# Kernel tuning notes

Measured on AMD Instinct MI355X. Metric: run time of the kernel, lower is better.

Reference implementation:

```python
import jax, jax.numpy as jnp
import numpy as np

N = 262144       # rows
D = 256          # feature dim
CLUSTER = 512    # number of clusters


def setup_inputs() -> dict:
    key = jax.random.key(0)
    k1, k2 = jax.random.split(key)
    matrix = jax.random.normal(k1, (N, D), dtype=jnp.float32)
    label = jax.random.randint(k2, (N,), 0, CLUSTER, dtype=jnp.int32)
    return {"matrix": matrix, "label": label}


def reference(matrix, label):
    # Segment-mean: scatter-add rows into their cluster, divide by counts.
    # (Intended math of the original per-row loop + count-normalize.)
    sums = jax.ops.segment_sum(matrix, label, num_segments=CLUSTER)            # [C, D]
    counts = jax.ops.segment_sum(
        jnp.ones((matrix.shape[0],), matrix.dtype), label, num_segments=CLUSTER
    )                                                                          # [C]
    centers = sums / jnp.maximum(counts, 1.0)[:, None]                         # [C, D]

    # torch.nn.functional.pdist: L2 distance over all unordered pairs i<j.
    iu, ju = jnp.triu_indices(CLUSTER, k=1)                                    # static [P]
    diff = centers[iu] - centers[ju]                                           # [P, D]
    sq = jnp.sum(diff * diff, axis=-1)                                         # [P]
    dist = jnp.sqrt(jnp.maximum(sq, 1e-12))                                    # eps-guard for sqrt grad
    return -jnp.mean(dist)
```

## Files before the change

### kernel.cpp

```cpp
#include <hip/hip_runtime.h>

#define NROWS   262144
#define DIM     256
#define CLUSTER 512
#define NPAIR   (CLUSTER * (CLUSTER - 1) / 2)
#define G       16
#define CPG     32
#define R       64
#define CHUNK   (NROWS / R)
#define PAIR_BLOCKS 2044

__global__ __launch_bounds__(256) void k_gather(const float* __restrict__ matrix,
                                                const int* __restrict__ label,
                                                float* __restrict__ partial,
                                                int* __restrict__ countpart) {
    int g = blockIdx.x & (G - 1);
    int r = blockIdx.x >> 4;
    int t = threadIdx.x;
    int w = t >> 6, lane = t & 63;
    int base = r * CHUNK;

    __shared__ unsigned short list[CHUNK];
    __shared__ int cnt[CPG];
    __shared__ int off[CPG + 1];
    __shared__ int cur[CPG];

    if (t < CPG) cnt[t] = 0;
    __syncthreads();

    for (int i = t; i < CHUNK; i += 256) {
        int lab = label[base + i];
        if ((lab >> 5) == g) atomicAdd(&cnt[lab & (CPG - 1)], 1);
    }
    __syncthreads();

    if (t == 0) {
        int s = 0;
        #pragma unroll
        for (int c = 0; c < CPG; ++c) { off[c] = s; cur[c] = s; s += cnt[c]; }
        off[CPG] = s;
    }
    __syncthreads();

    for (int i = t; i < CHUNK; i += 256) {
        int lab = label[base + i];
        if ((lab >> 5) == g) {
            int p = atomicAdd(&cur[lab & (CPG - 1)], 1);
            list[p] = (unsigned short)i;
        }
    }
    __syncthreads();

    #pragma unroll
    for (int q = 0; q < 8; ++q) {
        int cl = q * 4 + w;
        int s0 = off[cl], s1 = off[cl + 1];
        float ax = 0.f, ay = 0.f, az = 0.f, aw = 0.f;
        #pragma unroll 4
        for (int k = s0; k < s1; ++k) {
            int li = list[k];
            const float4* row = (const float4*)(matrix + (size_t)(base + li) * DIM);
            float4 v = row[lane];
            ax += v.x; ay += v.y; az += v.z; aw += v.w;
        }
        int c = g * CPG + cl;
        ((float4*)(partial + ((size_t)c * R + r) * DIM))[lane] =
            make_float4(ax, ay, az, aw);
    }
    if (t < CPG) countpart[r * CLUSTER + g * CPG + t] = cnt[t];
}

__global__ __launch_bounds__(256) void k_center(const float* __restrict__ partial,
                                                const int* __restrict__ countpart,
                                                float* __restrict__ centers) {
    int c = blockIdx.x, d = threadIdx.x;
    __shared__ float invc;
    if (d == 0) {
        int s = 0;
        for (int r = 0; r < R; ++r) s += countpart[r * CLUSTER + c];
        invc = 1.0f / (float)max(s, 1);
    }
    float acc = 0.f;
    const float* p = partial + (size_t)c * R * DIM + d;
    #pragma unroll 8
    for (int r = 0; r < R; ++r) acc += p[r * DIM];
    __syncthreads();
    centers[c * DIM + d] = acc * invc;
}

__device__ __forceinline__ long long tri_off(long long i) {
    return i * (2 * CLUSTER - i - 1) / 2;
}

__global__ __launch_bounds__(256) void k_pairs(const float* __restrict__ centers,
                                               float* __restrict__ partials) {
    int wave = threadIdx.x >> 6;
    int lane = threadIdx.x & 63;
    long long base = ((long long)blockIdx.x * 4 + wave) * 16;

    double sq = sqrt((double)((2LL * CLUSTER - 1) * (2LL * CLUSTER - 1) - 8 * base));
    int i = (int)(((2 * CLUSTER - 1) - sq) * 0.5);
    if (i < 0) i = 0;
    while (tri_off(i + 1) <= base) ++i;
    while (tri_off(i) > base) --i;
    int j = (int)(base - tri_off(i)) + i + 1;

    float wsum = 0.f;
    #pragma unroll 4
    for (int q = 0; q < 16; ++q) {
        const float4* ci = (const float4*)(centers + (size_t)i * DIM);
        const float4* cj = (const float4*)(centers + (size_t)j * DIM);
        float4 a = ci[lane], b = cj[lane];
        float dx = a.x - b.x, dy = a.y - b.y, dz = a.z - b.z, dw = a.w - b.w;
        float local = dx * dx + dy * dy + dz * dz + dw * dw;
        #pragma unroll
        for (int o = 32; o; o >>= 1) local += __shfl_xor(local, o, 64);
        wsum += sqrtf(fmaxf(local, 1e-12f));
        if (++j == CLUSTER) { ++i; j = i + 1; }
    }

    __shared__ float bsum[4];
    if (lane == 0) bsum[wave] = wsum;
    __syncthreads();
    if (threadIdx.x == 0)
        partials[blockIdx.x] = bsum[0] + bsum[1] + bsum[2] + bsum[3];
}

__global__ __launch_bounds__(256) void k_final(const float* __restrict__ partials, int nb,
                                               float* __restrict__ out) {
    __shared__ float s[256];
    float acc = 0.f;
    for (int i = threadIdx.x; i < nb; i += 256) acc += partials[i];
    s[threadIdx.x] = acc;
    __syncthreads();
    for (int d = 128; d; d >>= 1) {
        if (threadIdx.x < d) s[threadIdx.x] += s[threadIdx.x + d];
        __syncthreads();
    }
    if (threadIdx.x == 0) out[0] = -s[0] / (float)NPAIR;
}

extern "C" void kernel_launch(void* const* d_in, const int* in_sizes, int n_in,
                              void* d_out, int out_size, void* d_ws, size_t ws_size,
                              hipStream_t stream) {
    const float* matrix = (const float*)d_in[0];
    const int* label = (const int*)d_in[1];
    float* out = (float*)d_out;

    float* partial   = (float*)d_ws;
    float* centers   = partial + (size_t)CLUSTER * R * DIM;
    float* ppart     = centers + (size_t)CLUSTER * DIM;
    int*   countpart = (int*)(ppart + 4096);

    k_gather<<<G * R, 256, 0, stream>>>(matrix, label, partial, countpart);
    k_center<<<CLUSTER, 256, 0, stream>>>(partial, countpart, centers);
    k_pairs<<<PAIR_BLOCKS, 256, 0, stream>>>(centers, ppart);
    k_final<<<1, 256, 0, stream>>>(ppart, PAIR_BLOCKS, out);
}
```

Measured before the change: 402.0 us.

## Replace per-chunk partial sums with global atomic accumulation into cluster sums

The gather kernel now accumulates its per-cluster row sums straight into a global [C,D] buffer with float atomics, instead of writing a [C,R,D] partial array. The separate center reduction kernel becomes a simple elementwise normalize. A memset zeroes the sums and counts first, and empty clusters are skipped. This removes the 32 MB partial write and its re-read, at the cost of atomic contention (64 chunks per address), an extra memset launch, and a summation order that is no longer deterministic.

```diff
diff --git a/kernel.cpp b/kernel.cpp
--- a/kernel.cpp
+++ b/kernel.cpp
@@ -12,8 +12,8 @@
 
 __global__ __launch_bounds__(256) void k_gather(const float* __restrict__ matrix,
                                                 const int* __restrict__ label,
-                                                float* __restrict__ partial,
-                                                int* __restrict__ countpart) {
+                                                float* __restrict__ sums,
+                                                int* __restrict__ counts) {
     int g = blockIdx.x & (G - 1);
     int r = blockIdx.x >> 4;
     int t = threadIdx.x;
@@ -55,6 +55,7 @@
     for (int q = 0; q < 8; ++q) {
         int cl = q * 4 + w;
         int s0 = off[cl], s1 = off[cl + 1];
+        if (s0 == s1) continue;
         float ax = 0.f, ay = 0.f, az = 0.f, aw = 0.f;
         #pragma unroll 4
         for (int k = s0; k < s1; ++k) {
@@ -63,29 +64,24 @@
             float4 v = row[lane];
             ax += v.x; ay += v.y; az += v.z; aw += v.w;
         }
-        int c = g * CPG + cl;
-        ((float4*)(partial + ((size_t)c * R + r) * DIM))[lane] =
-            make_float4(ax, ay, az, aw);
+        float* dst = sums + ((size_t)(g * CPG + cl)) * DIM + lane * 4;
+        atomicAdd(dst + 0, ax);
+        atomicAdd(dst + 1, ay);
+        atomicAdd(dst + 2, az);
+        atomicAdd(dst + 3, aw);
     }
-    if (t < CPG) countpart[r * CLUSTER + g * CPG + t] = cnt[t];
+    if (t < CPG && cnt[t]) atomicAdd(&counts[g * CPG + t], cnt[t]);
 }
 
-__global__ __launch_bounds__(256) void k_center(const float* __restrict__ partial,
-                                                const int* __restrict__ countpart,
-                                                float* __restrict__ centers) {
-    int c = blockIdx.x, d = threadIdx.x;
-    __shared__ float invc;
-    if (d == 0) {
-        int s = 0;
-        for (int r = 0; r < R; ++r) s += countpart[r * CLUSTER + c];
-        invc = 1.0f / (float)max(s, 1);
-    }
-    float acc = 0.f;
-    const float* p = partial + (size_t)c * R * DIM + d;
-    #pragma unroll 8
-    for (int r = 0; r < R; ++r) acc += p[r * DIM];
-    __syncthreads();
-    centers[c * DIM + d] = acc * invc;
+__global__ __launch_bounds__(256) void k_norm(const float* __restrict__ sums,
+                                              const int* __restrict__ counts,
+                                              float* __restrict__ centers) {
+    int idx = blockIdx.x * 256 + threadIdx.x;
+    int c = idx >> 6;
+    float inv = 1.0f / (float)max(counts[c], 1);
+    float4 s = ((const float4*)sums)[idx];
+    s.x *= inv; s.y *= inv; s.z *= inv; s.w *= inv;
+    ((float4*)centers)[idx] = s;
 }
 
 __device__ __forceinline__ long long tri_off(long long i) {
@@ -147,13 +143,15 @@
     const int* label = (const int*)d_in[1];
     float* out = (float*)d_out;
 
-    float* partial   = (float*)d_ws;
-    float* centers   = partial + (size_t)CLUSTER * R * DIM;
-    float* ppart     = centers + (size_t)CLUSTER * DIM;
-    int*   countpart = (int*)(ppart + 4096);
+    float* sums    = (float*)d_ws;
+    int*   counts  = (int*)(sums + (size_t)CLUSTER * DIM);
+    float* centers = (float*)(counts + CLUSTER);
+    float* ppart   = centers + (size_t)CLUSTER * DIM;
 
-    k_gather<<<G * R, 256, 0, stream>>>(matrix, label, partial, countpart);
-    k_center<<<CLUSTER, 256, 0, stream>>>(partial, countpart, centers);
+    hipMemsetAsync(sums, 0, (size_t)CLUSTER * DIM * sizeof(float) + CLUSTER * sizeof(int),
+                   stream);
+    k_gather<<<G * R, 256, 0, stream>>>(matrix, label, sums, counts);
+    k_norm<<<CLUSTER * DIM / 4 / 256, 256, 0, stream>>>(sums, counts, centers);
     k_pairs<<<PAIR_BLOCKS, 256, 0, stream>>>(centers, ppart);
     k_final<<<1, 256, 0, stream>>>(ppart, PAIR_BLOCKS, out);
 }
```

Result: slower. 565.3 us (+40.6%).

## Software-prefetch gathered rows, vectorize label scans, fold final reduction into atomics

Applied to the files above, without the earlier changes.

The gather kernel now reads labels as int4 vectors, and each wave walks a contiguous run of 8 clusters with an 8-deep register prefetch ring of row loads. This keeps more global loads in flight and balances the per-wave work, which is meant to hide memory latency in the dominant gather phase. The count reduction in k_center now uses a wave shuffle instead of a serial loop. The final reduction kernel is removed: k_pairs block sums go directly into the output through float atomics after a memset. That saves a launch but makes the float summation order nondeterministic.

```diff
diff --git a/kernel.cpp b/kernel.cpp
--- a/kernel.cpp
+++ b/kernel.cpp
@@ -8,6 +8,7 @@
 #define CPG     32
 #define R       64
 #define CHUNK   (NROWS / R)
+#define PF      8
 #define PAIR_BLOCKS 2044
 
 __global__ __launch_bounds__(256) void k_gather(const float* __restrict__ matrix,
@@ -28,9 +29,13 @@
     if (t < CPG) cnt[t] = 0;
     __syncthreads();
 
-    for (int i = t; i < CHUNK; i += 256) {
-        int lab = label[base + i];
-        if ((lab >> 5) == g) atomicAdd(&cnt[lab & (CPG - 1)], 1);
+    const int4* lab4 = (const int4*)(label + base);
+    for (int i = t; i < CHUNK / 4; i += 256) {
+        int4 L = lab4[i];
+        if ((L.x >> 5) == g) atomicAdd(&cnt[L.x & (CPG - 1)], 1);
+        if ((L.y >> 5) == g) atomicAdd(&cnt[L.y & (CPG - 1)], 1);
+        if ((L.z >> 5) == g) atomicAdd(&cnt[L.z & (CPG - 1)], 1);
+        if ((L.w >> 5) == g) atomicAdd(&cnt[L.w & (CPG - 1)], 1);
     }
     __syncthreads();
 
@@ -42,30 +47,55 @@
     }
     __syncthreads();
 
-    for (int i = t; i < CHUNK; i += 256) {
-        int lab = label[base + i];
-        if ((lab >> 5) == g) {
-            int p = atomicAdd(&cur[lab & (CPG - 1)], 1);
-            list[p] = (unsigned short)i;
-        }
+    for (int i = t; i < CHUNK / 4; i += 256) {
+        int4 L = lab4[i];
+        int i4 = i * 4;
+        if ((L.x >> 5) == g) list[atomicAdd(&cur[L.x & (CPG - 1)], 1)] = (unsigned short)(i4 + 0);
+        if ((L.y >> 5) == g) list[atomicAdd(&cur[L.y & (CPG - 1)], 1)] = (unsigned short)(i4 + 1);
+        if ((L.z >> 5) == g) list[atomicAdd(&cur[L.z & (CPG - 1)], 1)] = (unsigned short)(i4 + 2);
+        if ((L.w >> 5) == g) list[atomicAdd(&cur[L.w & (CPG - 1)], 1)] = (unsigned short)(i4 + 3);
     }
     __syncthreads();
 
+    int c0 = w * 8;
+    int lo = off[c0], hi = off[c0 + 8];
+    int seg = c0;
+    int nextb = off[seg + 1];
+    float ax = 0.f, ay = 0.f, az = 0.f, aq = 0.f;
+
+    float4 pv[PF];
     #pragma unroll
-    for (int q = 0; q < 8; ++q) {
-        int cl = q * 4 + w;
-        int s0 = off[cl], s1 = off[cl + 1];
-        float ax = 0.f, ay = 0.f, az = 0.f, aw = 0.f;
-        #pragma unroll 4
-        for (int k = s0; k < s1; ++k) {
-            int li = list[k];
-            const float4* row = (const float4*)(matrix + (size_t)(base + li) * DIM);
-            float4 v = row[lane];
-            ax += v.x; ay += v.y; az += v.z; aw += v.w;
+    for (int d = 0; d < PF; ++d) {
+        int k = lo + d;
+        int li = (k < hi) ? (int)list[k] : 0;
+        pv[d] = ((const float4*)(matrix + (size_t)(base + li) * DIM))[lane];
+    }
+
+    for (int k0 = lo; k0 < hi; k0 += PF) {
+        #pragma unroll
+        for (int d = 0; d < PF; ++d) {
+            int k = k0 + d;
+            if (k >= hi) break;
+            float4 v = pv[d];
+            int kn = k + PF;
+            if (kn < hi) {
+                int li = list[kn];
+                pv[d] = ((const float4*)(matrix + (size_t)(base + li) * DIM))[lane];
+            }
+            while (k >= nextb) {
+                ((float4*)(partial + ((size_t)(g * CPG + seg) * R + r) * DIM))[lane] =
+                    make_float4(ax, ay, az, aq);
+                ax = ay = az = aq = 0.f;
+                ++seg; nextb = off[seg + 1];
+            }
+            ax += v.x; ay += v.y; az += v.z; aq += v.w;
         }
-        int c = g * CPG + cl;
-        ((float4*)(partial + ((size_t)c * R + r) * DIM))[lane] =
-            make_float4(ax, ay, az, aw);
+    }
+    while (seg < c0 + 8) {
+        ((float4*)(partial + ((size_t)(g * CPG + seg) * R + r) * DIM))[lane] =
+            make_float4(ax, ay, az, aq);
+        ax = ay = az = aq = 0.f;
+        ++seg;
     }
     if (t < CPG) countpart[r * CLUSTER + g * CPG + t] = cnt[t];
 }
@@ -73,19 +103,20 @@
 __global__ __launch_bounds__(256) void k_center(const float* __restrict__ partial,
                                                 const int* __restrict__ countpart,
                                                 float* __restrict__ centers) {
-    int c = blockIdx.x, d = threadIdx.x;
-    __shared__ float invc;
-    if (d == 0) {
-        int s = 0;
-        for (int r = 0; r < R; ++r) s += countpart[r * CLUSTER + c];
-        invc = 1.0f / (float)max(s, 1);
+    int c = blockIdx.x, t = threadIdx.x;
+    __shared__ float sinv;
+    if (t < 64) {
+        int cv = countpart[t * CLUSTER + c];
+        #pragma unroll
+        for (int o = 32; o; o >>= 1) cv += __shfl_down(cv, o, 64);
+        if (t == 0) sinv = 1.0f / (float)max(cv, 1);
     }
     float acc = 0.f;
-    const float* p = partial + (size_t)c * R * DIM + d;
+    const float* p = partial + (size_t)c * R * DIM + t;
     #pragma unroll 8
     for (int r = 0; r < R; ++r) acc += p[r * DIM];
     __syncthreads();
-    centers[c * DIM + d] = acc * invc;
+    centers[c * DIM + t] = acc * sinv;
 }
 
 __device__ __forceinline__ long long tri_off(long long i) {
@@ -93,7 +124,7 @@
 }
 
 __global__ __launch_bounds__(256) void k_pairs(const float* __restrict__ centers,
-                                               float* __restrict__ partials) {
+                                               float* __restrict__ out) {
     int wave = threadIdx.x >> 6;
     int lane = threadIdx.x & 63;
     long long base = ((long long)blockIdx.x * 4 + wave) * 16;
@@ -123,21 +154,7 @@
     if (lane == 0) bsum[wave] = wsum;
     __syncthreads();
     if (threadIdx.x == 0)
-        partials[blockIdx.x] = bsum[0] + bsum[1] + bsum[2] + bsum[3];
-}
-
-__global__ __launch_bounds__(256) void k_final(const float* __restrict__ partials, int nb,
-                                               float* __restrict__ out) {
-    __shared__ float s[256];
-    float acc = 0.f;
-    for (int i = threadIdx.x; i < nb; i += 256) acc += partials[i];
-    s[threadIdx.x] = acc;
-    __syncthreads();
-    for (int d = 128; d; d >>= 1) {
-        if (threadIdx.x < d) s[threadIdx.x] += s[threadIdx.x + d];
-        __syncthreads();
-    }
-    if (threadIdx.x == 0) out[0] = -s[0] / (float)NPAIR;
+        atomicAdd(out, (bsum[0] + bsum[1] + bsum[2] + bsum[3]) * (-1.0f / (float)NPAIR));
 }
 
 extern "C" void kernel_launch(void* const* d_in, const int* in_sizes, int n_in,
@@ -149,11 +166,10 @@
 
     float* partial   = (float*)d_ws;
     float* centers   = partial + (size_t)CLUSTER * R * DIM;
-    float* ppart     = centers + (size_t)CLUSTER * DIM;
-    int*   countpart = (int*)(ppart + 4096);
+    int*   countpart = (int*)(centers + (size_t)CLUSTER * DIM);
 
+    hipMemsetAsync(out, 0, sizeof(float), stream);
     k_gather<<<G * R, 256, 0, stream>>>(matrix, label, partial, countpart);
     k_center<<<CLUSTER, 256, 0, stream>>>(partial, countpart, centers);
-    k_pairs<<<PAIR_BLOCKS, 256, 0, stream>>>(centers, ppart);
-    k_final<<<1, 256, 0, stream>>>(ppart, PAIR_BLOCKS, out);
+    k_pairs<<<PAIR_BLOCKS, 256, 0, stream>>>(centers, out);
 }
```

Result: slower. 420.8 us (+4.7%).
